# Kernel tuning notes

Hardware: AMD Instinct MI355X
Metric: run time of the kernel (lower is better)

Reference implementation:

```python
import jax, jax.numpy as jnp
import numpy as np

WINDOW_SIZE = 11
SIGMA = 1.5
C1 = 0.01 ** 2
C2 = 0.03 ** 2
LAMBDA_DSSIM = 0.2


def _gaussian_window(channel):
    x = jnp.arange(WINDOW_SIZE, dtype=jnp.float32)
    g = jnp.exp(-((x - WINDOW_SIZE // 2) ** 2) / (2.0 * SIGMA ** 2))
    g = g / g.sum()
    w2d = jnp.outer(g, g)  # [ws, ws]
    # depthwise kernel: [O=C, I=1, ws, ws]
    return jnp.broadcast_to(w2d[None, None], (channel, 1, WINDOW_SIZE, WINDOW_SIZE))


def _dwconv(x, window, channel):
    # x: [1, C, H, W]; same padding ws//2, depthwise (groups=C)
    pad = WINDOW_SIZE // 2
    return jax.lax.conv_general_dilated(
        x, window,
        window_strides=(1, 1),
        padding=((pad, pad), (pad, pad)),
        dimension_numbers=("NCHW", "OIHW", "NCHW"),
        feature_group_count=channel,
    )


def _ssim_mean(img1, img2):
    # img1, img2: [C, H, W]
    channel = img1.shape[0]
    window = _gaussian_window(channel).astype(img1.dtype)
    a = img1[None]  # [1, C, H, W]
    b = img2[None]

    mu1 = _dwconv(a, window, channel)
    mu2 = _dwconv(b, window, channel)
    mu1_sq = mu1 * mu1
    mu2_sq = mu2 * mu2
    mu1_mu2 = mu1 * mu2
    sigma1_sq = _dwconv(a * a, window, channel) - mu1_sq
    sigma2_sq = _dwconv(b * b, window, channel) - mu2_sq
    sigma12 = _dwconv(a * b, window, channel) - mu1_mu2

    ssim_map = ((2 * mu1_mu2 + C1) * (2 * sigma12 + C2)) / (
        (mu1_sq + mu2_sq + C1) * (sigma1_sq + sigma2_sq + C2))
    return ssim_map.mean()


def setup_inputs() -> dict:
    key = jax.random.key(0)
    k1, k2 = jax.random.split(key)
    shape = (3, 2160, 3840)
    pred = jax.random.uniform(k1, shape, dtype=jnp.float32)
    target = jax.random.uniform(k2, shape, dtype=jnp.float32)
    return {"pred": pred, "target": target}


def reference(pred, target):
    l1 = jnp.abs(pred - target).mean()
    ssim_val = _ssim_mean(pred, target)
    return (1.0 - LAMBDA_DSSIM) * l1 + LAMBDA_DSSIM * (1.0 - ssim_val)
```

## Files before the change

### kernel.cpp

```cpp
#include <hip/hip_runtime.h>
#include <math.h>

#define WSZ 11
#define PAD 5
#define TX 32
#define TY 24
#define NY 6
#define IY (TY + 2*PAD)
#define RX 4
#define NTASK0 (IY * 8)
#define NTASK1 (TY * 8)
#define SEG (RX + 2*PAD)
#define RY 3
#define SA 33

typedef float v2f __attribute__((ext_vector_type(2)));

struct W11 { float w[WSZ]; };

__global__ __launch_bounds__(256, 4) void ssim_l1_kernel(
    const float* __restrict__ pred, const float* __restrict__ targ,
    W11 wt, float2* __restrict__ partials)
{
    constexpr int H = 2160, W = 3840;
    __shared__ float4 sH[2][IY][SA];

    const int c    = blockIdx.z;
    const int gx0  = blockIdx.x * TX;
    const int base = blockIdx.y * (TY * NY);
    const size_t plane = (size_t)H * W;
    const float* p = pred + (size_t)c * plane;
    const float* t = targ + (size_t)c * plane;

    const int tid = threadIdx.x;
    v2f loss_acc = {0.f, 0.f};
    const float C1v = 0.0001f, C2v = 0.0009f;

    const int oxB  = tid & 31;
    const int oy0B = (tid >> 5) * RY;
    const bool xfast = (blockIdx.x >= 1) && (blockIdx.x <= (W / TX) - 2);

    auto phaseA = [&](float4 (*__restrict__ dst)[SA], const int s) {
        const int ntask  = (s == 0) ? NTASK0 : NTASK1;
        const int rowoff = (s == 0) ? 0 : 2 * PAD;
        const int gyA    = base + TY * s - PAD;
        for (int task = tid; task < ntask; task += 256) {
            const int r  = task >> 3;
            const int cx = task & 7;
            const int rr = rowoff + r;
            const int gy = gyA + rr;
            const int gxs = gx0 + cx * RX - PAD;
            const bool rowok   = (gy >= 0) && (gy < H);
            const bool own_row = (gy >= base) && (gy < base + TY * NY);

            float4 P[5], T[5];
            if (rowok && xfast) {
                const float4* p4 = (const float4*)(p + (size_t)gy * W + (gxs - 3));
                const float4* t4 = (const float4*)(t + (size_t)gy * W + (gxs - 3));
                #pragma unroll
                for (int i = 0; i < 5; ++i) { P[i] = p4[i]; T[i] = t4[i]; }
            } else if (rowok) {
                const size_t rowoff2 = (size_t)gy * W;
                #pragma unroll
                for (int i = 0; i < 5; ++i) {
                    float pe[4], te[4];
                    #pragma unroll
                    for (int q = 0; q < 4; ++q) {
                        int gx = gxs - 3 + 4 * i + q;
                        bool ok = (gx >= 0) && (gx < W);
                        pe[q] = ok ? p[rowoff2 + gx] : 0.f;
                        te[q] = ok ? t[rowoff2 + gx] : 0.f;
                    }
                    P[i] = make_float4(pe[0], pe[1], pe[2], pe[3]);
                    T[i] = make_float4(te[0], te[1], te[2], te[3]);
                }
            } else {
                #pragma unroll
                for (int i = 0; i < 5; ++i) {
                    P[i] = make_float4(0.f, 0.f, 0.f, 0.f);
                    T[i] = make_float4(0.f, 0.f, 0.f, 0.f);
                }
            }

            v2f h_sd[RX], h_qq[RX];
            #pragma unroll
            for (int j = 0; j < RX; ++j) {
                h_sd[j] = (v2f){0.f, 0.f};
                h_qq[j] = (v2f){0.f, 0.f};
            }
            #pragma unroll
            for (int e = 0; e < SEG; ++e) {
                const int ii = (e + 3) >> 2, qq = (e + 3) & 3;
                const float pe = (qq == 0) ? P[ii].x : (qq == 1) ? P[ii].y
                                : (qq == 2) ? P[ii].z : P[ii].w;
                const float te = (qq == 0) ? T[ii].x : (qq == 1) ? T[ii].y
                                : (qq == 2) ? T[ii].z : T[ii].w;
                v2f vsd; vsd.x = pe + te; vsd.y = pe - te;
                const v2f vsq = vsd * vsd;
                #pragma unroll
                for (int j = 0; j < RX; ++j) {
                    const int k = e - j;
                    if (k >= 0 && k < WSZ) {
                        const float wv = wt.w[k];
                        h_sd[j] += wv * vsd;
                        h_qq[j] += wv * vsq;
                    }
                }
                if (e >= PAD && e < PAD + RX && own_row)
                    loss_acc.y += fabsf(vsd.y);
            }
            const int xb = cx * RX;
            #pragma unroll
            for (int j = 0; j < RX; ++j)
                dst[rr][xb + j] = make_float4(h_sd[j].x, h_sd[j].y,
                                              h_qq[j].x, h_qq[j].y);
        }
    };

    phaseA(sH[0], 0);
    __syncthreads();

    for (int s = 0; s < NY; ++s) {
        float4 (*cur)[SA] = sH[s & 1];
        float4 (*nxt)[SA] = sH[(s & 1) ^ 1];

        if (s < NY - 1) {
            for (int i = tid; i < 2 * PAD * TX; i += 256) {
                const int dr = i >> 5, cc = i & 31;
                nxt[dr][cc] = cur[dr + TY][cc];
            }
            phaseA(nxt, s + 1);
        }

        {
            v2f mu[RY], qq[RY];
            #pragma unroll
            for (int j = 0; j < RY; ++j) {
                mu[j] = (v2f){0.f, 0.f};
                qq[j] = (v2f){0.f, 0.f};
            }
            #pragma unroll
            for (int k = 0; k < RY + 2 * PAD; ++k) {
                const float4 f = cur[oy0B + k][oxB];
                v2f fsd; fsd.x = f.x; fsd.y = f.y;
                v2f fsq; fsq.x = f.z; fsq.y = f.w;
                #pragma unroll
                for (int j = 0; j < RY; ++j) {
                    const int kk = k - j;
                    if (kk >= 0 && kk < WSZ) {
                        const float wv = wt.w[kk];
                        mu[j] += wv * fsd;
                        qq[j] += wv * fsq;
                    }
                }
            }
            #pragma unroll
            for (int j = 0; j < RY; ++j) {
                const v2f musq = mu[j] * mu[j];
                const v2f rr2  = qq[j] - musq;
                const float a    = 0.5f * (musq.x - musq.y) + C1v;
                const float b    = 0.5f * (rr2.x - rr2.y) + C2v;
                const float cden = 0.5f * (musq.x + musq.y) + C1v;
                const float dden = 0.5f * (rr2.x + rr2.y) + C2v;
                loss_acc.x += (a * b) * __builtin_amdgcn_rcpf(cden * dden);
            }
        }
        __syncthreads();
    }

    #pragma unroll
    for (int off = 32; off > 0; off >>= 1) {
        loss_acc.x += __shfl_down(loss_acc.x, off, 64);
        loss_acc.y += __shfl_down(loss_acc.y, off, 64);
    }
    __shared__ float red[2][4];
    const int lane = tid & 63;
    const int wid  = tid >> 6;
    if (lane == 0) { red[0][wid] = loss_acc.x; red[1][wid] = loss_acc.y; }
    __syncthreads();
    if (tid == 0) {
        const float sv = red[0][0] + red[0][1] + red[0][2] + red[0][3];
        const float lv = red[1][0] + red[1][1] + red[1][2] + red[1][3];
        const int bid = (blockIdx.z * gridDim.y + blockIdx.y) * gridDim.x + blockIdx.x;
        partials[bid] = make_float2(sv, lv);
    }
}

__global__ __launch_bounds__(256) void finalize_kernel(
    const float2* __restrict__ partials, int n,
    float* __restrict__ out, double invN)
{
    const int tid = threadIdx.x;
    double s = 0.0, l = 0.0;
    for (int i = tid; i < n; i += 256) {
        float2 v = partials[i];
        s += (double)v.x;
        l += (double)v.y;
    }
    #pragma unroll
    for (int off = 32; off > 0; off >>= 1) {
        s += __shfl_down(s, off, 64);
        l += __shfl_down(l, off, 64);
    }
    __shared__ double rs[4], rl[4];
    const int lane = tid & 63, wid = tid >> 6;
    if (lane == 0) { rs[wid] = s; rl[wid] = l; }
    __syncthreads();
    if (tid == 0) {
        const double st = rs[0] + rs[1] + rs[2] + rs[3];
        const double lt = rl[0] + rl[1] + rl[2] + rl[3];
        out[0] = (float)(0.8 * lt * invN + 0.2 * (1.0 - st * invN));
    }
}

extern "C" void kernel_launch(void* const* d_in, const int* in_sizes, int n_in,
                              void* d_out, int out_size, void* d_ws, size_t ws_size,
                              hipStream_t stream)
{
    const float* pred = (const float*)d_in[0];
    const float* targ = (const float*)d_in[1];
    float* out = (float*)d_out;
    float2* partials = (float2*)d_ws;

    const int C = 3, H = 2160, W = 3840;

    W11 wt;
    double g[WSZ], sg = 0.0;
    for (int i = 0; i < WSZ; ++i) {
        double d = (double)i - (WSZ / 2);
        g[i] = exp(-(d * d) / (2.0 * 1.5 * 1.5));
        sg += g[i];
    }
    for (int i = 0; i < WSZ; ++i) wt.w[i] = (float)(g[i] / sg);

    dim3 grid(W / TX, H / (TY * NY), C);
    ssim_l1_kernel<<<grid, 256, 0, stream>>>(pred, targ, wt, partials);

    const int nblocks = (W / TX) * (H / (TY * NY)) * C;
    double invN = 1.0 / ((double)C * (double)H * (double)W);
    finalize_kernel<<<1, 256, 0, stream>>>(partials, nblocks, out, invN);
}
```

Baseline: 261.0 us.

## Specialize warps into horizontal-conv producers and vertical-conv consumers with smaller strips

Splits the 256-thread block into two halves. Threads 0-127 compute the horizontal convolution for the next strip. Threads 128-255 compute the vertical convolution and SSIM for the current strip. Strip height drops from 24 to 16 rows and strip count rises from 6 to 9, so each producer thread handles exactly one row-segment task. The goal is to overlap the global-load-bound horizontal pass with the LDS-bound vertical pass inside one block, but each phase now uses only half the threads, which risks load imbalance between the two roles.

```diff
diff --git a/kernel.cpp b/kernel.cpp
--- a/kernel.cpp
+++ b/kernel.cpp
@@ -4,14 +4,12 @@
 #define WSZ 11
 #define PAD 5
 #define TX 32
-#define TY 24
-#define NY 6
+#define TY 16
+#define NY 9
 #define IY (TY + 2*PAD)
 #define RX 4
-#define NTASK0 (IY * 8)
-#define NTASK1 (TY * 8)
 #define SEG (RX + 2*PAD)
-#define RY 3
+#define RYC 4
 #define SA 33
 
 typedef float v2f __attribute__((ext_vector_type(2)));
@@ -35,117 +33,112 @@
     const int tid = threadIdx.x;
     v2f loss_acc = {0.f, 0.f};
     const float C1v = 0.0001f, C2v = 0.0009f;
-
-    const int oxB  = tid & 31;
-    const int oy0B = (tid >> 5) * RY;
     const bool xfast = (blockIdx.x >= 1) && (blockIdx.x <= (W / TX) - 2);
 
-    auto phaseA = [&](float4 (*__restrict__ dst)[SA], const int s) {
-        const int ntask  = (s == 0) ? NTASK0 : NTASK1;
-        const int rowoff = (s == 0) ? 0 : 2 * PAD;
-        const int gyA    = base + TY * s - PAD;
-        for (int task = tid; task < ntask; task += 256) {
-            const int r  = task >> 3;
-            const int cx = task & 7;
-            const int rr = rowoff + r;
-            const int gy = gyA + rr;
-            const int gxs = gx0 + cx * RX - PAD;
-            const bool rowok   = (gy >= 0) && (gy < H);
-            const bool own_row = (gy >= base) && (gy < base + TY * NY);
-
-            float4 P[5], T[5];
-            if (rowok && xfast) {
-                const float4* p4 = (const float4*)(p + (size_t)gy * W + (gxs - 3));
-                const float4* t4 = (const float4*)(t + (size_t)gy * W + (gxs - 3));
+    auto hconv = [&](float4 (*__restrict__ dst)[SA], const int rr,
+                     const int gy, const int cx) {
+        const int gxs = gx0 + cx * RX - PAD;
+        const bool rowok   = (gy >= 0) && (gy < H);
+        const bool own_row = (gy >= base) && (gy < base + TY * NY);
+
+        float4 P[5], T[5];
+        if (rowok && xfast) {
+            const float4* p4 = (const float4*)(p + (size_t)gy * W + (gxs - 3));
+            const float4* t4 = (const float4*)(t + (size_t)gy * W + (gxs - 3));
+            #pragma unroll
+            for (int i = 0; i < 5; ++i) { P[i] = p4[i]; T[i] = t4[i]; }
+        } else if (rowok) {
+            const size_t rowoff2 = (size_t)gy * W;
+            #pragma unroll
+            for (int i = 0; i < 5; ++i) {
+                float pe[4], te[4];
                 #pragma unroll
-                for (int i = 0; i < 5; ++i) { P[i] = p4[i]; T[i] = t4[i]; }
-            } else if (rowok) {
-                const size_t rowoff2 = (size_t)gy * W;
-                #pragma unroll
-                for (int i = 0; i < 5; ++i) {
-                    float pe[4], te[4];
-                    #pragma unroll
-                    for (int q = 0; q < 4; ++q) {
-                        int gx = gxs - 3 + 4 * i + q;
-                        bool ok = (gx >= 0) && (gx < W);
-                        pe[q] = ok ? p[rowoff2 + gx] : 0.f;
-                        te[q] = ok ? t[rowoff2 + gx] : 0.f;
-                    }
-                    P[i] = make_float4(pe[0], pe[1], pe[2], pe[3]);
-                    T[i] = make_float4(te[0], te[1], te[2], te[3]);
-                }
-            } else {
-                #pragma unroll
-                for (int i = 0; i < 5; ++i) {
-                    P[i] = make_float4(0.f, 0.f, 0.f, 0.f);
-                    T[i] = make_float4(0.f, 0.f, 0.f, 0.f);
-                }
-            }
-
-            v2f h_sd[RX], h_qq[RX];
+                for (int q = 0; q < 4; ++q) {
+                    int gx = gxs - 3 + 4 * i + q;
+                    bool ok = (gx >= 0) && (gx < W);
+                    pe[q] = ok ? p[rowoff2 + gx] : 0.f;
+                    te[q] = ok ? t[rowoff2 + gx] : 0.f;
+                }
+                P[i] = make_float4(pe[0], pe[1], pe[2], pe[3]);
+                T[i] = make_float4(te[0], te[1], te[2], te[3]);
+            }
+        } else {
+            #pragma unroll
+            for (int i = 0; i < 5; ++i) {
+                P[i] = make_float4(0.f, 0.f, 0.f, 0.f);
+                T[i] = make_float4(0.f, 0.f, 0.f, 0.f);
+            }
+        }
+
+        v2f h_sd[RX], h_qq[RX];
+        #pragma unroll
+        for (int j = 0; j < RX; ++j) {
+            h_sd[j] = (v2f){0.f, 0.f};
+            h_qq[j] = (v2f){0.f, 0.f};
+        }
+        #pragma unroll
+        for (int e = 0; e < SEG; ++e) {
+            const int ii = (e + 3) >> 2, qq = (e + 3) & 3;
+            const float pe = (qq == 0) ? P[ii].x : (qq == 1) ? P[ii].y
+                            : (qq == 2) ? P[ii].z : P[ii].w;
+            const float te = (qq == 0) ? T[ii].x : (qq == 1) ? T[ii].y
+                            : (qq == 2) ? T[ii].z : T[ii].w;
+            v2f vsd; vsd.x = pe + te; vsd.y = pe - te;
+            const v2f vsq = vsd * vsd;
             #pragma unroll
             for (int j = 0; j < RX; ++j) {
-                h_sd[j] = (v2f){0.f, 0.f};
-                h_qq[j] = (v2f){0.f, 0.f};
-            }
-            #pragma unroll
-            for (int e = 0; e < SEG; ++e) {
-                const int ii = (e + 3) >> 2, qq = (e + 3) & 3;
-                const float pe = (qq == 0) ? P[ii].x : (qq == 1) ? P[ii].y
-                                : (qq == 2) ? P[ii].z : P[ii].w;
-                const float te = (qq == 0) ? T[ii].x : (qq == 1) ? T[ii].y
-                                : (qq == 2) ? T[ii].z : T[ii].w;
-                v2f vsd; vsd.x = pe + te; vsd.y = pe - te;
-                const v2f vsq = vsd * vsd;
-                #pragma unroll
-                for (int j = 0; j < RX; ++j) {
-                    const int k = e - j;
-                    if (k >= 0 && k < WSZ) {
-                        const float wv = wt.w[k];
-                        h_sd[j] += wv * vsd;
-                        h_qq[j] += wv * vsq;
-                    }
-                }
-                if (e >= PAD && e < PAD + RX && own_row)
-                    loss_acc.y += fabsf(vsd.y);
-            }
-            const int xb = cx * RX;
-            #pragma unroll
-            for (int j = 0; j < RX; ++j)
-                dst[rr][xb + j] = make_float4(h_sd[j].x, h_sd[j].y,
-                                              h_qq[j].x, h_qq[j].y);
-        }
+                const int k = e - j;
+                if (k >= 0 && k < WSZ) {
+                    const float wv = wt.w[k];
+                    h_sd[j] += wv * vsd;
+                    h_qq[j] += wv * vsq;
+                }
+            }
+            if (e >= PAD && e < PAD + RX && own_row)
+                loss_acc.y += fabsf(vsd.y);
+        }
+        const int xb = cx * RX;
+        #pragma unroll
+        for (int j = 0; j < RX; ++j)
+            dst[rr][xb + j] = make_float4(h_sd[j].x, h_sd[j].y,
+                                          h_qq[j].x, h_qq[j].y);
     };
 
-    phaseA(sH[0], 0);
+    if (tid < IY * 8) {
+        const int r = tid >> 3, cx = tid & 7;
+        hconv(sH[0], r, base - PAD + r, cx);
+    }
     __syncthreads();
 
     for (int s = 0; s < NY; ++s) {
         float4 (*cur)[SA] = sH[s & 1];
         float4 (*nxt)[SA] = sH[(s & 1) ^ 1];
 
-        if (s < NY - 1) {
-            for (int i = tid; i < 2 * PAD * TX; i += 256) {
-                const int dr = i >> 5, cc = i & 31;
-                nxt[dr][cc] = cur[dr + TY][cc];
-            }
-            phaseA(nxt, s + 1);
-        }
-
-        {
-            v2f mu[RY], qq[RY];
-            #pragma unroll
-            for (int j = 0; j < RY; ++j) {
+        if (tid < 128) {
+            if (s < NY - 1) {
+                for (int i = tid; i < 2 * PAD * TX; i += 128) {
+                    const int dr = i >> 5, cc = i & 31;
+                    nxt[dr][cc] = cur[TY + dr][cc];
+                }
+                const int r = tid >> 3, cx = tid & 7;
+                hconv(nxt, 10 + r, base - PAD + TY * (s + 1) + 10 + r, cx);
+            }
+        } else {
+            const int oxB = tid & 31;
+            const int oy0 = ((tid >> 5) & 3) * RYC;
+            v2f mu[RYC], qq[RYC];
+            #pragma unroll
+            for (int j = 0; j < RYC; ++j) {
                 mu[j] = (v2f){0.f, 0.f};
                 qq[j] = (v2f){0.f, 0.f};
             }
             #pragma unroll
-            for (int k = 0; k < RY + 2 * PAD; ++k) {
-                const float4 f = cur[oy0B + k][oxB];
+            for (int k = 0; k < RYC + 2 * PAD; ++k) {
+                const float4 f = cur[oy0 + k][oxB];
                 v2f fsd; fsd.x = f.x; fsd.y = f.y;
                 v2f fsq; fsq.x = f.z; fsq.y = f.w;
                 #pragma unroll
-                for (int j = 0; j < RY; ++j) {
+                for (int j = 0; j < RYC; ++j) {
                     const int kk = k - j;
                     if (kk >= 0 && kk < WSZ) {
                         const float wv = wt.w[kk];
@@ -155,7 +148,7 @@
                 }
             }
             #pragma unroll
-            for (int j = 0; j < RY; ++j) {
+            for (int j = 0; j < RYC; ++j) {
                 const v2f musq = mu[j] * mu[j];
                 const v2f rr2  = qq[j] - musq;
                 const float a    = 0.5f * (musq.x - musq.y) + C1v;
```

Result: faster. 252.1 us (-3.4%).
